# Optimization experiments

Measured on AMD Instinct MI355X. Metric: run time of the kernel, lower is better.

## Reference

```python
import jax, jax.numpy as jnp
import numpy as np

BN_EPS = 1e-5


def _gin_layer(x, src, dst, ew, eps, Wa, ba, Wb, bb, gamma, beta):
    # scatter-add aggregation: sum_j w_ij * x_j into node i
    msg = x[src] * ew[:, None]                       # [E, F]
    agg = jax.ops.segment_sum(msg, dst, num_segments=x.shape[0])  # [N, F]
    h = (1.0 + eps) * x + agg
    # MLP: Linear -> ReLU -> Linear -> BN(batch stats) -> ReLU
    h = jax.nn.relu(h @ Wa + ba)
    h = h @ Wb + bb
    mean = jnp.mean(h, axis=0)
    var = jnp.var(h, axis=0)
    h = (h - mean) * jax.lax.rsqrt(var + BN_EPS) * gamma + beta
    return jax.nn.relu(h)


def setup_inputs() -> dict:
    key = jax.random.key(0)
    N, E, F, H, L = 100000, 1600000, 128, 64, 3
    ks = jax.random.split(key, 12)
    x = jax.random.normal(ks[0], (N, F), dtype=jnp.float32)
    edge_index = jax.random.randint(ks[1], (2, E), 0, N, dtype=jnp.int64)
    edge_weight = jax.random.uniform(ks[2], (E,), dtype=jnp.float32)
    s = 0.05
    return {
        "x": x,
        "edge_index": edge_index,
        "edge_weight": edge_weight,
        # layer 1 (in_features -> hidden)
        "eps1": jnp.zeros((), jnp.float32),
        "W1a": jax.random.normal(ks[3], (F, H), jnp.float32) * s,
        "b1a": jnp.zeros((H,), jnp.float32),
        "W1b": jax.random.normal(ks[4], (H, H), jnp.float32) * s,
        "b1b": jnp.zeros((H,), jnp.float32),
        "g1": jnp.ones((H,), jnp.float32),
        "be1": jnp.zeros((H,), jnp.float32),
        # layers 2..L (hidden -> hidden), stacked on leading axis
        "epss": jnp.zeros((L - 1,), jnp.float32),
        "Wsa": jax.random.normal(ks[5], (L - 1, H, H), jnp.float32) * s,
        "bsa": jnp.zeros((L - 1, H), jnp.float32),
        "Wsb": jax.random.normal(ks[6], (L - 1, H, H), jnp.float32) * s,
        "bsb": jnp.zeros((L - 1, H), jnp.float32),
        "gs": jnp.ones((L - 1, H), jnp.float32),
        "bes": jnp.zeros((L - 1, H), jnp.float32),
    }


def reference(x, edge_index, edge_weight, eps1, W1a, b1a, W1b, b1b, g1, be1,
              epss, Wsa, bsa, Wsb, bsb, gs, bes):
    src, dst = edge_index[0], edge_index[1]
    h = _gin_layer(x, src, dst, edge_weight, eps1, W1a, b1a, W1b, b1b, g1, be1)
    for i in range(Wsa.shape[0]):
        h_new = _gin_layer(h, src, dst, edge_weight, epss[i],
                           Wsa[i], bsa[i], Wsb[i], bsb[i], gs[i], bes[i])
        h = h + h_new  # residual merge
    return h
```

## Files before the change

### kernel.cpp

```cpp
#include <hip/hip_runtime.h>

#define BN_EPS 1e-5f

typedef __attribute__((ext_vector_type(8))) short bf16x8;
typedef __attribute__((ext_vector_type(4))) float f32x4;

__device__ __forceinline__ unsigned short f32_to_bf16(float f) {
    unsigned u = __float_as_uint(f);
    u += 0x7fffu + ((u >> 16) & 1u);
    return (unsigned short)(u >> 16);
}
__device__ __forceinline__ float bf16_lo(unsigned v) { return __uint_as_float(v << 16); }
__device__ __forceinline__ float bf16_hi(unsigned v) { return __uint_as_float(v & 0xffff0000u); }

#define EW_SCALE (1.0f / 32767.0f)

__global__ __launch_bounds__(256) void scan_part1(
    const int* __restrict__ deg, int* __restrict__ blockSums, int N)
{
    __shared__ int sm[256];
    int t = threadIdx.x;
    int i0 = blockIdx.x * 512 + t * 2;
    int a = (i0     < N) ? deg[i0]     : 0;
    int b = (i0 + 1 < N) ? deg[i0 + 1] : 0;
    sm[t] = a + b;
    __syncthreads();
    for (int off = 128; off > 0; off >>= 1) {
        if (t < off) sm[t] += sm[t + off];
        __syncthreads();
    }
    if (t == 0) blockSums[blockIdx.x] = sm[0];
}

__global__ __launch_bounds__(256) void scan_part3(
    const int* __restrict__ deg, const int* __restrict__ blockSums,
    int* __restrict__ row_start, int NB, int N, int E)
{
    __shared__ int sb[256];
    __shared__ int sm[256];
    int t = threadIdx.x;

    sb[t] = (t < NB) ? blockSums[t] : 0;
    __syncthreads();
    for (int off = 1; off < 256; off <<= 1) {
        int v = (t >= off) ? sb[t - off] : 0;
        __syncthreads();
        sb[t] += v;
        __syncthreads();
    }
    const int boff = (blockIdx.x > 0) ? sb[blockIdx.x - 1] : 0;

    int i0 = blockIdx.x * 512 + t * 2;
    int a = (i0     < N) ? deg[i0]     : 0;
    int b = (i0 + 1 < N) ? deg[i0 + 1] : 0;
    sm[t] = a + b;
    __syncthreads();
    for (int off = 1; off < 256; off <<= 1) {
        int v = (t >= off) ? sm[t - off] : 0;
        __syncthreads();
        sm[t] += v;
        __syncthreads();
    }
    int excl = boff + ((t > 0) ? sm[t - 1] : 0);
    if (i0 < N)     row_start[i0]     = excl;
    if (i0 + 1 < N) row_start[i0 + 1] = excl + a;
    if (blockIdx.x == 0 && t == 0) row_start[N] = E;
}

__global__ __launch_bounds__(256) void fill_pass2(
    const int* __restrict__ src, const int* __restrict__ dst,
    const float* __restrict__ ew, const int* __restrict__ rank,
    const int* __restrict__ row_start, unsigned* __restrict__ einfo, int E)
{
    int i = blockIdx.x * 256 + threadIdx.x;
    if (i < E) {
        int pos = row_start[dst[i]] + rank[i];
        unsigned q = (unsigned)__float2int_rn(ew[i] * 32767.0f);
        einfo[pos] = ((unsigned)src[i] << 15) | q;
    }
}

__global__ __launch_bounds__(256) void prep_wfrag(
    const float* __restrict__ W1a, const float* __restrict__ W1b,
    const float* __restrict__ Wsa, const float* __restrict__ Wsb,
    unsigned short* __restrict__ wf, int* __restrict__ deg,
    float* __restrict__ stats3, int N, int nW)
{
    int z = blockIdx.x * 256 + threadIdx.x;
    if (z < N) deg[z] = 0;
    if (z < 384) stats3[z] = 0.f;

    int bid = blockIdx.x;
    if (bid >= nW) return;
    const float* src; unsigned short* dst; int KS, chunk;
    if (bid < 4)      { src = W1a; dst = wf;        KS = 4; chunk = bid; }
    else if (bid < 6) { src = W1b; dst = wf + 8192; KS = 2; chunk = bid - 4; }
    else {
        int t = bid - 6;
        int layer = t >> 2;
        int wh = (t >> 1) & 1;
        chunk = t & 1;
        src = (wh ? Wsb : Wsa) + (size_t)layer * 4096;
        dst = wf + 12288 + layer * 8192 + wh * 4096;
        KS = 2;
    }
    int base = chunk * 2048;
    for (int e = base + threadIdx.x; e < base + 2048; e += 256) {
        int j  = e & 7;
        int l  = (e >> 3) & 63;
        int nk = e >> 9;
        int ks = nk % KS, n = nk / KS;
        int k  = ks * 32 + ((l >> 4) << 3) + j;
        int c  = n * 16 + (l & 15);
        dst[e] = f32_to_bf16(src[k * 64 + c]);
    }
}

template<int KS, int MODE, bool BF16OUT, bool STATS>
__global__ __launch_bounds__(256) void gemm_mfma(
    const void* __restrict__ Ain, const unsigned short* __restrict__ wfrag,
    const float* __restrict__ bias, void* __restrict__ out,
    float* __restrict__ statsOut,
    const float* __restrict__ statsIn, const float* __restrict__ g,
    const float* __restrict__ be, const float* __restrict__ res,
    float* __restrict__ hout, int N,
    const int* __restrict__ rdst, int* __restrict__ rdeg,
    int* __restrict__ rrank, int rE, int gblocks)
{
    constexpr int K   = KS * 32;
    constexpr int LDA = K + 8;
    __shared__ __align__(16) unsigned short sA[64 * LDA];
    __shared__ float sab[128];

    const int tid = threadIdx.x;
    if ((int)blockIdx.x >= gblocks) {
        int i = (blockIdx.x - gblocks) * 256 + tid;
        if (i < rE) rrank[i] = atomicAdd(&rdeg[rdst[i]], 1);
        return;
    }
    const int bid = blockIdx.x;

    if (MODE == 2) {
        if (tid < 64) {
            float invN = 1.0f / (float)N;
            float mean = statsIn[tid] * invN;
            float var  = statsIn[64 + tid] * invN - mean * mean;
            float a = g[tid] * rsqrtf(var + BN_EPS);
            sab[tid]      = a;
            sab[64 + tid] = be[tid] - mean * a;
        }
        __syncthreads();
    }

    const int w  = tid >> 6;
    const int l  = tid & 63;
    const int lr = l & 15;
    const int lg = l >> 4;
    const int ntiles = (N + 63) >> 6;
    const bf16x8* wg = (const bf16x8*)wfrag;

    float csAcc[4] = {0.f, 0.f, 0.f, 0.f};
    float cqAcc[4] = {0.f, 0.f, 0.f, 0.f};

    for (int tile = bid; tile < ntiles; tile += gblocks) {
        const int r0 = tile * 64;

        if (MODE == 1) {
            const uint4* Au = (const uint4*)Ain;
            constexpr int C16 = K / 8;
            for (int i = tid; i < 64 * C16; i += 256) {
                int r = i / C16, c = i % C16;
                uint4 v = make_uint4(0u, 0u, 0u, 0u);
                if (r0 + r < N) v = Au[(size_t)(r0 + r) * C16 + c];
                *reinterpret_cast<uint4*>(&sA[r * LDA + c * 8]) = v;
            }
        } else {
            const float* Af = (const float*)Ain;
            constexpr int C4 = K / 4;
            for (int i = tid; i < 64 * C4; i += 256) {
                int r = i / C4, c4 = i % C4;
                int gr = r0 + r;
                float4 v = make_float4(0.f, 0.f, 0.f, 0.f);
                if (gr < N) {
                    v = reinterpret_cast<const float4*>(Af + (size_t)gr * K)[c4];
                    if (MODE == 2) {
                        int l0 = c4 * 4;
                        v.x = fmaxf(fmaf(v.x, sab[l0 + 0], sab[64 + l0 + 0]), 0.f);
                        v.y = fmaxf(fmaf(v.y, sab[l0 + 1], sab[64 + l0 + 1]), 0.f);
                        v.z = fmaxf(fmaf(v.z, sab[l0 + 2], sab[64 + l0 + 2]), 0.f);
                        v.w = fmaxf(fmaf(v.w, sab[l0 + 3], sab[64 + l0 + 3]), 0.f);
                        if (res) {
                            float4 rv = reinterpret_cast<const float4*>(res + (size_t)gr * K)[c4];
                            v.x += rv.x; v.y += rv.y; v.z += rv.z; v.w += rv.w;
                        }
                        reinterpret_cast<float4*>(hout + (size_t)gr * K)[c4] = v;
                    }
                }
                ushort4 pk;
                pk.x = f32_to_bf16(v.x); pk.y = f32_to_bf16(v.y);
                pk.z = f32_to_bf16(v.z); pk.w = f32_to_bf16(v.w);
                *reinterpret_cast<ushort4*>(&sA[r * LDA + c4 * 4]) = pk;
            }
        }
        __syncthreads();

        f32x4 acc0 = {0.f,0.f,0.f,0.f}, acc1 = {0.f,0.f,0.f,0.f};
        f32x4 acc2 = {0.f,0.f,0.f,0.f}, acc3 = {0.f,0.f,0.f,0.f};

        #pragma unroll
        for (int ks = 0; ks < KS; ++ks) {
            bf16x8 af = *reinterpret_cast<const bf16x8*>(
                &sA[(w * 16 + lr) * LDA + ks * 32 + lg * 8]);
            bf16x8 b0 = wg[(0 * KS + ks) * 64 + l];
            bf16x8 b1 = wg[(1 * KS + ks) * 64 + l];
            bf16x8 b2 = wg[(2 * KS + ks) * 64 + l];
            bf16x8 b3 = wg[(3 * KS + ks) * 64 + l];
            acc0 = __builtin_amdgcn_mfma_f32_16x16x32_bf16(af, b0, acc0, 0, 0, 0);
            acc1 = __builtin_amdgcn_mfma_f32_16x16x32_bf16(af, b1, acc1, 0, 0, 0);
            acc2 = __builtin_amdgcn_mfma_f32_16x16x32_bf16(af, b2, acc2, 0, 0, 0);
            acc3 = __builtin_amdgcn_mfma_f32_16x16x32_bf16(af, b3, acc3, 0, 0, 0);
        }

        const int rlocal = w * 16 + lg * 4;
        float v[4][4];
        #pragma unroll
        for (int n = 0; n < 4; ++n) {
            float bv = bias ? bias[n * 16 + lr] : 0.f;
            f32x4 a = (n == 0) ? acc0 : (n == 1) ? acc1 : (n == 2) ? acc2 : acc3;
            #pragma unroll
            for (int j = 0; j < 4; ++j) {
                float vv = a[j] + bv;
                v[n][j] = vv;
                if (STATS && (r0 + rlocal + j < N)) {
                    csAcc[n] += vv; cqAcc[n] += vv * vv;
                }
            }
        }

        __syncthreads();

        if (BF16OUT) {
            #pragma unroll
            for (int n = 0; n < 4; ++n)
                #pragma unroll
                for (int j = 0; j < 4; ++j)
                    sA[(rlocal + j) * 72 + n * 16 + lr] = f32_to_bf16(v[n][j]);
            __syncthreads();
            unsigned short* o = (unsigned short*)out;
            for (int i = tid; i < 64 * 8; i += 256) {
                int r = i >> 3, q = i & 7;
                if (r0 + r < N)
                    *reinterpret_cast<uint4*>(o + (size_t)(r0 + r) * 64 + q * 8) =
                        *reinterpret_cast<const uint4*>(&sA[r * 72 + q * 8]);
            }
        } else {
            float* o = (float*)out;
            float* sAf = reinterpret_cast<float*>(sA);
            #pragma unroll
            for (int half = 0; half < 2; ++half) {
                if ((w >> 1) == half) {
                    #pragma unroll
                    for (int n = 0; n < 4; ++n)
                        #pragma unroll
                        for (int j = 0; j < 4; ++j)
                            sAf[((w & 1) * 16 + lg * 4 + j) * 68 + n * 16 + lr] = v[n][j];
                }
                __syncthreads();
                for (int i = tid; i < 32 * 16; i += 256) {
                    int r = i >> 4, c4 = i & 15;
                    int gr = r0 + half * 32 + r;
                    if (gr < N)
                        *reinterpret_cast<float4*>(o + (size_t)gr * 64 + c4 * 4) =
                            *reinterpret_cast<const float4*>(&sAf[r * 68 + c4 * 4]);
                }
                __syncthreads();
            }
        }
        __syncthreads();
    }

    if (STATS) {
        float* red = reinterpret_cast<float*>(sA);
        int gg = w * 4 + lg;
        #pragma unroll
        for (int n = 0; n < 4; ++n) red[gg * 64 + n * 16 + lr] = csAcc[n];
        __syncthreads();
        if (tid < 64) {
            float s = 0.f;
            #pragma unroll
            for (int g2 = 0; g2 < 16; ++g2) s += red[g2 * 64 + tid];
            atomicAdd(&statsOut[tid], s);
        }
        __syncthreads();
        #pragma unroll
        for (int n = 0; n < 4; ++n) red[gg * 64 + n * 16 + lr] = cqAcc[n];
        __syncthreads();
        if (tid < 64) {
            float q = 0.f;
            #pragma unroll
            for (int g2 = 0; g2 < 16; ++g2) q += red[g2 * 64 + tid];
            atomicAdd(&statsOut[64 + tid], q);
        }
    }
}

__global__ __launch_bounds__(256) void aggmid_kernel(
    const unsigned* __restrict__ yu,
    const int* __restrict__ row_start,
    const unsigned* __restrict__ einfo,
    const float* __restrict__ epsp,
    const float* __restrict__ ba,
    unsigned* __restrict__ midu, int N)
{
    const int lane = threadIdx.x & 63;
    const int q    = lane >> 4;
    const int u    = lane & 15;
    int w  = (blockIdx.x * 256 + threadIdx.x) >> 6;
    const int nw = (gridDim.x * 256) >> 6;
    const float eps1 = 1.0f + epsp[0];
    const float4 bal = *reinterpret_cast<const float4*>(ba + 4 * u);

    for (int r = w; r < N; r += nw) {
        const int rs = row_start[r];
        const int re = row_start[r + 1];

        float A0=0.f,A1=0.f,A2=0.f,A3=0.f, B0=0.f,B1=0.f,B2=0.f,B3=0.f;
        float C0=0.f,C1=0.f,C2=0.f,C3=0.f, D0=0.f,D1=0.f,D2=0.f,D3=0.f;
        int j = rs;
        for (; j + 16 <= re; j += 16) {
            const int b = j + q * 4;
            unsigned p0 = einfo[b + 0], p1 = einfo[b + 1];
            unsigned p2 = einfo[b + 2], p3 = einfo[b + 3];
            uint2 y0 = *reinterpret_cast<const uint2*>(&yu[(size_t)(p0 >> 15) * 32 + 2 * u]);
            uint2 y1 = *reinterpret_cast<const uint2*>(&yu[(size_t)(p1 >> 15) * 32 + 2 * u]);
            uint2 y2 = *reinterpret_cast<const uint2*>(&yu[(size_t)(p2 >> 15) * 32 + 2 * u]);
            uint2 y3 = *reinterpret_cast<const uint2*>(&yu[(size_t)(p3 >> 15) * 32 + 2 * u]);
            float w0 = (float)(p0 & 0x7FFFu) * EW_SCALE;
            float w1 = (float)(p1 & 0x7FFFu) * EW_SCALE;
            float w2 = (float)(p2 & 0x7FFFu) * EW_SCALE;
            float w3 = (float)(p3 & 0x7FFFu) * EW_SCALE;
            A0 = fmaf(w0, bf16_lo(y0.x), A0); A1 = fmaf(w0, bf16_hi(y0.x), A1);
            A2 = fmaf(w0, bf16_lo(y0.y), A2); A3 = fmaf(w0, bf16_hi(y0.y), A3);
            B0 = fmaf(w1, bf16_lo(y1.x), B0); B1 = fmaf(w1, bf16_hi(y1.x), B1);
            B2 = fmaf(w1, bf16_lo(y1.y), B2); B3 = fmaf(w1, bf16_hi(y1.y), B3);
            C0 = fmaf(w2, bf16_lo(y2.x), C0); C1 = fmaf(w2, bf16_hi(y2.x), C1);
            C2 = fmaf(w2, bf16_lo(y2.y), C2); C3 = fmaf(w2, bf16_hi(y2.y), C3);
            D0 = fmaf(w3, bf16_lo(y3.x), D0); D1 = fmaf(w3, bf16_hi(y3.x), D1);
            D2 = fmaf(w3, bf16_lo(y3.y), D2); D3 = fmaf(w3, bf16_hi(y3.y), D3);
        }
        for (; j + 4 <= re; j += 4) {
            unsigned p = einfo[j + q];
            uint2 y = *reinterpret_cast<const uint2*>(&yu[(size_t)(p >> 15) * 32 + 2 * u]);
            float wv = (float)(p & 0x7FFFu) * EW_SCALE;
            A0 = fmaf(wv, bf16_lo(y.x), A0); A1 = fmaf(wv, bf16_hi(y.x), A1);
            A2 = fmaf(wv, bf16_lo(y.y), A2); A3 = fmaf(wv, bf16_hi(y.y), A3);
        }
        if (j < re) {
            int e = j + q;
            bool valid = e < re;
            unsigned p = einfo[valid ? e : rs];
            float wv = valid ? (float)(p & 0x7FFFu) * EW_SCALE : 0.f;
            uint2 y = *reinterpret_cast<const uint2*>(&yu[(size_t)(p >> 15) * 32 + 2 * u]);
            B0 = fmaf(wv, bf16_lo(y.x), B0); B1 = fmaf(wv, bf16_hi(y.x), B1);
            B2 = fmaf(wv, bf16_lo(y.y), B2); B3 = fmaf(wv, bf16_hi(y.y), B3);
        }
        float s0 = (A0 + B0) + (C0 + D0);
        float s1 = (A1 + B1) + (C1 + D1);
        float s2 = (A2 + B2) + (C2 + D2);
        float s3 = (A3 + B3) + (C3 + D3);
        s0 += __shfl_xor(s0, 16); s0 += __shfl_xor(s0, 32);
        s1 += __shfl_xor(s1, 16); s1 += __shfl_xor(s1, 32);
        s2 += __shfl_xor(s2, 16); s2 += __shfl_xor(s2, 32);
        s3 += __shfl_xor(s3, 16); s3 += __shfl_xor(s3, 32);

        uint2 sv = *reinterpret_cast<const uint2*>(&yu[(size_t)r * 32 + 2 * u]);
        float m0 = fmaf(eps1, bf16_lo(sv.x), s0) + bal.x;
        float m1 = fmaf(eps1, bf16_hi(sv.x), s1) + bal.y;
        float m2 = fmaf(eps1, bf16_lo(sv.y), s2) + bal.z;
        float m3 = fmaf(eps1, bf16_hi(sv.y), s3) + bal.w;
        if (q == 0) {
            uint2 pk;
            pk.x = (unsigned)f32_to_bf16(fmaxf(m0, 0.f))
                 | ((unsigned)f32_to_bf16(fmaxf(m1, 0.f)) << 16);
            pk.y = (unsigned)f32_to_bf16(fmaxf(m2, 0.f))
                 | ((unsigned)f32_to_bf16(fmaxf(m3, 0.f)) << 16);
            *reinterpret_cast<uint2*>(&midu[(size_t)r * 32 + 2 * u]) = pk;
        }
    }
}

template<int RES>
__global__ __launch_bounds__(256) void bn_apply(
    const float* __restrict__ h2, const float* __restrict__ stats,
    const float* __restrict__ g, const float* __restrict__ be,
    const float* res, float* out, int N, int n4)
{
    __shared__ float sab[128];
    int t = threadIdx.x;
    if (t < 64) {
        float invN = 1.0f / (float)N;
        float mean = stats[t] * invN;
        float var  = stats[64 + t] * invN - mean * mean;
        float a = g[t] * rsqrtf(var + BN_EPS);
        sab[t]      = a;
        sab[64 + t] = be[t] - mean * a;
    }
    __syncthreads();

    int i = blockIdx.x * blockDim.x + t;
    int stride = gridDim.x * blockDim.x;
    for (; i < n4; i += stride) {
        float4 v = reinterpret_cast<const float4*>(h2)[i];
        int l0 = (i * 4) & 63;
        float4 o;
        o.x = fmaxf(fmaf(v.x, sab[l0 + 0], sab[64 + l0 + 0]), 0.f);
        o.y = fmaxf(fmaf(v.y, sab[l0 + 1], sab[64 + l0 + 1]), 0.f);
        o.z = fmaxf(fmaf(v.z, sab[l0 + 2], sab[64 + l0 + 2]), 0.f);
        o.w = fmaxf(fmaf(v.w, sab[l0 + 3], sab[64 + l0 + 3]), 0.f);
        if (RES) {
            float4 rv = reinterpret_cast<const float4*>(res)[i];
            o.x += rv.x; o.y += rv.y; o.z += rv.z; o.w += rv.w;
        }
        reinterpret_cast<float4*>(out)[i] = o;
    }
}

extern "C" void kernel_launch(void* const* d_in, const int* in_sizes, int n_in,
                              void* d_out, int out_size, void* d_ws, size_t ws_size,
                              hipStream_t stream)
{
    const float* x    = (const float*)d_in[0];
    const int*   ei   = (const int*)  d_in[1];
    const float* ew   = (const float*)d_in[2];
    const float* eps1 = (const float*)d_in[3];
    const float* W1a  = (const float*)d_in[4];
    const float* b1a  = (const float*)d_in[5];
    const float* W1b  = (const float*)d_in[6];
    const float* b1b  = (const float*)d_in[7];
    const float* g1   = (const float*)d_in[8];
    const float* be1  = (const float*)d_in[9];
    const float* epss = (const float*)d_in[10];
    const float* Wsa  = (const float*)d_in[11];
    const float* bsa  = (const float*)d_in[12];
    const float* Wsb  = (const float*)d_in[13];
    const float* bsb  = (const float*)d_in[14];
    const float* gs   = (const float*)d_in[15];
    const float* bes  = (const float*)d_in[16];

    const int N   = in_sizes[0] / 128;
    const int E   = in_sizes[2];
    const int Lm1 = in_sizes[10];
    const int* src  = ei;
    const int* dstp = ei + E;

    char* ws = (char*)d_ws;
    size_t off = 0;
    unsigned* einfo = (unsigned*)(ws + off); off += (size_t)E * 4;
    float* regA  = (float*)(ws + off);   off += (size_t)N * 128 * 4;
    unsigned* ybf = (unsigned*)(ws + off); off += (size_t)N * 32 * 4;
    int*   rank  = (int*)  (ws + off);   off += (size_t)E * 4;
    int*   deg   = (int*)  (ws + off);   off += (size_t)N * 4;
    int*   row_start = (int*)(ws + off); off += (size_t)(N + 1) * 4;
    float* stats3 = (float*)(ws + off);  off += 384 * 4;
    int*   blockSums = (int*)(ws + off); off += 256 * 4;
    off = (off + 15) & ~(size_t)15;
    unsigned short* wf = (unsigned short*)(ws + off);
    float* outp  = (float*)d_out;
    float* bufY  = regA;
    unsigned* midu = (unsigned*)(regA + (size_t)N * 64);

    const int n4   = N * 64 / 4;
    const int NB   = (N + 511) / 512;
    const int EB   = (E + 255) / 256;
    const int nW   = 6 + 4 * Lm1;
    const int PREP_B = (N + 255) / 256;
    const int NT   = (N + 63) / 64;
    const int GBS  = 1024;

    prep_wfrag<<<PREP_B, 256, 0, stream>>>(W1a, W1b, Wsa, Wsb, wf, deg, stats3, N, nW);

    gemm_mfma<4, 0, true, false><<<1024 + EB, 256, 0, stream>>>(
        x, wf, nullptr, ybf, nullptr, nullptr, nullptr, nullptr, nullptr, nullptr, N,
        dstp, deg, rank, E, 1024);

    scan_part1<<<NB, 256, 0, stream>>>(deg, blockSums, N);
    scan_part3<<<NB, 256, 0, stream>>>(deg, blockSums, row_start, NB, N, E);
    fill_pass2<<<EB, 256, 0, stream>>>(src, dstp, ew, rank, row_start, einfo, E);

    aggmid_kernel<<<2048, 256, 0, stream>>>(ybf, row_start, einfo, eps1, b1a, midu, N);
    gemm_mfma<2, 1, false, true><<<GBS, 256, 0, stream>>>(
        midu, wf + 8192, b1b, bufY, stats3, nullptr, nullptr, nullptr, nullptr, nullptr, N,
        nullptr, nullptr, nullptr, 0, GBS);

    const float* pg  = g1;
    const float* pbe = be1;
    const float* resp = nullptr;
    for (int i = 0; i < Lm1; ++i) {
        const unsigned short* wfAi = wf + 12288 + i * 8192;
        const unsigned short* wfBi = wf + 12288 + i * 8192 + 4096;
        gemm_mfma<2, 2, true, false><<<NT, 256, 0, stream>>>(
            bufY, wfAi, nullptr, ybf, nullptr, stats3 + i * 128, pg, pbe, resp, outp, N,
            nullptr, nullptr, nullptr, 0, NT);
        aggmid_kernel<<<2048, 256, 0, stream>>>(
            ybf, row_start, einfo, epss + i, bsa + (size_t)i * 64, midu, N);
        gemm_mfma<2, 1, false, true><<<GBS, 256, 0, stream>>>(
            midu, wfBi, bsb + (size_t)i * 64, bufY, stats3 + (i + 1) * 128,
            nullptr, nullptr, nullptr, nullptr, nullptr, N,
            nullptr, nullptr, nullptr, 0, GBS);
        pg  = gs  + (size_t)i * 64;
        pbe = bes + (size_t)i * 64;
        resp = outp;
    }

    if (Lm1 > 0)
        bn_apply<1><<<2048, 256, 0, stream>>>(bufY, stats3 + Lm1 * 128, pg, pbe, outp, outp, N, n4);
    else
        bn_apply<0><<<2048, 256, 0, stream>>>(bufY, stats3, pg, pbe, nullptr, outp, N, n4);
}
```

Before: 401.5 us.

## Fuse second MLP linear and BN stats into aggregation kernel

New measurement: 544.9 us. 35.7% more time.

```diff
diff --git a/kernel.cpp b/kernel.cpp
--- a/kernel.cpp
+++ b/kernel.cpp
@@ -81,8 +81,7 @@
 }
 
 __global__ __launch_bounds__(256) void prep_wfrag(
-    const float* __restrict__ W1a, const float* __restrict__ W1b,
-    const float* __restrict__ Wsa, const float* __restrict__ Wsb,
+    const float* __restrict__ W1a, const float* __restrict__ Wsa,
     unsigned short* __restrict__ wf, int* __restrict__ deg,
     float* __restrict__ stats3, int N, int nW)
 {
@@ -93,15 +92,13 @@
     int bid = blockIdx.x;
     if (bid >= nW) return;
     const float* src; unsigned short* dst; int KS, chunk;
-    if (bid < 4)      { src = W1a; dst = wf;        KS = 4; chunk = bid; }
-    else if (bid < 6) { src = W1b; dst = wf + 8192; KS = 2; chunk = bid - 4; }
+    if (bid < 4) { src = W1a; dst = wf; KS = 4; chunk = bid; }
     else {
-        int t = bid - 6;
-        int layer = t >> 2;
-        int wh = (t >> 1) & 1;
+        int t = bid - 4;
+        int layer = t >> 1;
         chunk = t & 1;
-        src = (wh ? Wsb : Wsa) + (size_t)layer * 4096;
-        dst = wf + 12288 + layer * 8192 + wh * 4096;
+        src = Wsa + (size_t)layer * 4096;
+        dst = wf + 8192 + layer * 4096;
         KS = 2;
     }
     int base = chunk * 2048;
@@ -116,11 +113,10 @@
     }
 }
 
-template<int KS, int MODE, bool BF16OUT, bool STATS>
+template<int KS, int MODE>
 __global__ __launch_bounds__(256) void gemm_mfma(
     const void* __restrict__ Ain, const unsigned short* __restrict__ wfrag,
-    const float* __restrict__ bias, void* __restrict__ out,
-    float* __restrict__ statsOut,
+    void* __restrict__ out,
     const float* __restrict__ statsIn, const float* __restrict__ g,
     const float* __restrict__ be, const float* __restrict__ res,
     float* __restrict__ hout, int N,
@@ -159,22 +155,10 @@
     const int ntiles = (N + 63) >> 6;
     const bf16x8* wg = (const bf16x8*)wfrag;
 
-    float csAcc[4] = {0.f, 0.f, 0.f, 0.f};
-    float cqAcc[4] = {0.f, 0.f, 0.f, 0.f};
-
     for (int tile = bid; tile < ntiles; tile += gblocks) {
         const int r0 = tile * 64;
 
-        if (MODE == 1) {
-            const uint4* Au = (const uint4*)Ain;
-            constexpr int C16 = K / 8;
-            for (int i = tid; i < 64 * C16; i += 256) {
-                int r = i / C16, c = i % C16;
-                uint4 v = make_uint4(0u, 0u, 0u, 0u);
-                if (r0 + r < N) v = Au[(size_t)(r0 + r) * C16 + c];
-                *reinterpret_cast<uint4*>(&sA[r * LDA + c * 8]) = v;
-            }
-        } else {
+        {
             const float* Af = (const float*)Ain;
             constexpr int C4 = K / 4;
             for (int i = tid; i < 64 * C4; i += 256) {
@@ -225,100 +209,62 @@
         float v[4][4];
         #pragma unroll
         for (int n = 0; n < 4; ++n) {
-            float bv = bias ? bias[n * 16 + lr] : 0.f;
             f32x4 a = (n == 0) ? acc0 : (n == 1) ? acc1 : (n == 2) ? acc2 : acc3;
             #pragma unroll
-            for (int j = 0; j < 4; ++j) {
-                float vv = a[j] + bv;
-                v[n][j] = vv;
-                if (STATS && (r0 + rlocal + j < N)) {
-                    csAcc[n] += vv; cqAcc[n] += vv * vv;
-                }
-            }
-        }
-
-        __syncthreads();
-
-        if (BF16OUT) {
+            for (int j = 0; j < 4; ++j) v[n][j] = a[j];
+        }
+
+        __syncthreads();
+
+        #pragma unroll
+        for (int n = 0; n < 4; ++n)
             #pragma unroll
-            for (int n = 0; n < 4; ++n)
-                #pragma unroll
-                for (int j = 0; j < 4; ++j)
-                    sA[(rlocal + j) * 72 + n * 16 + lr] = f32_to_bf16(v[n][j]);
-            __syncthreads();
-            unsigned short* o = (unsigned short*)out;
-            for (int i = tid; i < 64 * 8; i += 256) {
-                int r = i >> 3, q = i & 7;
-                if (r0 + r < N)
-                    *reinterpret_cast<uint4*>(o + (size_t)(r0 + r) * 64 + q * 8) =
-                        *reinterpret_cast<const uint4*>(&sA[r * 72 + q * 8]);
-            }
-        } else {
-            float* o = (float*)out;
-            float* sAf = reinterpret_cast<float*>(sA);
-            #pragma unroll
-            for (int half = 0; half < 2; ++half) {
-                if ((w >> 1) == half) {
-                    #pragma unroll
-                    for (int n = 0; n < 4; ++n)
-                        #pragma unroll
-                        for (int j = 0; j < 4; ++j)
-                            sAf[((w & 1) * 16 + lg * 4 + j) * 68 + n * 16 + lr] = v[n][j];
-                }
-                __syncthreads();
-                for (int i = tid; i < 32 * 16; i += 256) {
-                    int r = i >> 4, c4 = i & 15;
-                    int gr = r0 + half * 32 + r;
-                    if (gr < N)
-                        *reinterpret_cast<float4*>(o + (size_t)gr * 64 + c4 * 4) =
-                            *reinterpret_cast<const float4*>(&sAf[r * 68 + c4 * 4]);
-                }
-                __syncthreads();
-            }
-        }
-        __syncthreads();
-    }
-
-    if (STATS) {
-        float* red = reinterpret_cast<float*>(sA);
-        int gg = w * 4 + lg;
-        #pragma unroll
-        for (int n = 0; n < 4; ++n) red[gg * 64 + n * 16 + lr] = csAcc[n];
-        __syncthreads();
-        if (tid < 64) {
-            float s = 0.f;
-            #pragma unroll
-            for (int g2 = 0; g2 < 16; ++g2) s += red[g2 * 64 + tid];
-            atomicAdd(&statsOut[tid], s);
-        }
-        __syncthreads();
-        #pragma unroll
-        for (int n = 0; n < 4; ++n) red[gg * 64 + n * 16 + lr] = cqAcc[n];
-        __syncthreads();
-        if (tid < 64) {
-            float q = 0.f;
-            #pragma unroll
-            for (int g2 = 0; g2 < 16; ++g2) q += red[g2 * 64 + tid];
-            atomicAdd(&statsOut[64 + tid], q);
-        }
-    }
-}
-
-__global__ __launch_bounds__(256) void aggmid_kernel(
+            for (int j = 0; j < 4; ++j)
+                sA[(rlocal + j) * 72 + n * 16 + lr] = f32_to_bf16(v[n][j]);
+        __syncthreads();
+        unsigned short* o = (unsigned short*)out;
+        for (int i = tid; i < 64 * 8; i += 256) {
+            int r = i >> 3, q = i & 7;
+            if (r0 + r < N)
+                *reinterpret_cast<uint4*>(o + (size_t)(r0 + r) * 64 + q * 8) =
+                    *reinterpret_cast<const uint4*>(&sA[r * 72 + q * 8]);
+        }
+        __syncthreads();
+    }
+}
+
+__global__ __launch_bounds__(256) void agg_mlp_kernel(
     const unsigned* __restrict__ yu,
     const int* __restrict__ row_start,
     const unsigned* __restrict__ einfo,
     const float* __restrict__ epsp,
     const float* __restrict__ ba,
-    unsigned* __restrict__ midu, int N)
-{
-    const int lane = threadIdx.x & 63;
+    const float* __restrict__ Wb,
+    const float* __restrict__ bb,
+    float* __restrict__ h2out,
+    float* __restrict__ statsOut, int N)
+{
+    __shared__ float sWb[64 * 64];
+    __shared__ float rowbuf[4][64];
+    __shared__ float sred[4][64];
+
+    const int tid  = threadIdx.x;
+    const int lane = tid & 63;
+    const int wid  = tid >> 6;
     const int q    = lane >> 4;
     const int u    = lane & 15;
-    int w  = (blockIdx.x * 256 + threadIdx.x) >> 6;
+
+    for (int i = tid; i < 1024; i += 256)
+        reinterpret_cast<float4*>(sWb)[i] = reinterpret_cast<const float4*>(Wb)[i];
+    __syncthreads();
+
+    int w  = (blockIdx.x * 256 + tid) >> 6;
     const int nw = (gridDim.x * 256) >> 6;
     const float eps1 = 1.0f + epsp[0];
     const float4 bal = *reinterpret_cast<const float4*>(ba + 4 * u);
+    const float bb_l = bb[lane];
+
+    float csA = 0.f, cqA = 0.f;
 
     for (int r = w; r < N; r += nw) {
         const int rs = row_start[r];
@@ -374,18 +320,42 @@
         s3 += __shfl_xor(s3, 16); s3 += __shfl_xor(s3, 32);
 
         uint2 sv = *reinterpret_cast<const uint2*>(&yu[(size_t)r * 32 + 2 * u]);
-        float m0 = fmaf(eps1, bf16_lo(sv.x), s0) + bal.x;
-        float m1 = fmaf(eps1, bf16_hi(sv.x), s1) + bal.y;
-        float m2 = fmaf(eps1, bf16_lo(sv.y), s2) + bal.z;
-        float m3 = fmaf(eps1, bf16_hi(sv.y), s3) + bal.w;
-        if (q == 0) {
-            uint2 pk;
-            pk.x = (unsigned)f32_to_bf16(fmaxf(m0, 0.f))
-                 | ((unsigned)f32_to_bf16(fmaxf(m1, 0.f)) << 16);
-            pk.y = (unsigned)f32_to_bf16(fmaxf(m2, 0.f))
-                 | ((unsigned)f32_to_bf16(fmaxf(m3, 0.f)) << 16);
-            *reinterpret_cast<uint2*>(&midu[(size_t)r * 32 + 2 * u]) = pk;
-        }
+        float m0 = fmaxf(fmaf(eps1, bf16_lo(sv.x), s0) + bal.x, 0.f);
+        float m1 = fmaxf(fmaf(eps1, bf16_hi(sv.x), s1) + bal.y, 0.f);
+        float m2 = fmaxf(fmaf(eps1, bf16_lo(sv.y), s2) + bal.z, 0.f);
+        float m3 = fmaxf(fmaf(eps1, bf16_hi(sv.y), s3) + bal.w, 0.f);
+
+        if (q == 0)
+            *reinterpret_cast<float4*>(&rowbuf[wid][4 * u]) =
+                make_float4(m0, m1, m2, m3);
+
+        float acc = bb_l;
+        #pragma unroll 4
+        for (int k = 0; k < 64; k += 4) {
+            float4 m = *reinterpret_cast<const float4*>(&rowbuf[wid][k]);
+            acc = fmaf(m.x, sWb[(k + 0) * 64 + lane], acc);
+            acc = fmaf(m.y, sWb[(k + 1) * 64 + lane], acc);
+            acc = fmaf(m.z, sWb[(k + 2) * 64 + lane], acc);
+            acc = fmaf(m.w, sWb[(k + 3) * 64 + lane], acc);
+        }
+        h2out[(size_t)r * 64 + lane] = acc;
+        csA += acc;
+        cqA += acc * acc;
+    }
+
+    __syncthreads();
+    sred[wid][lane] = csA;
+    __syncthreads();
+    if (tid < 64) {
+        float s = sred[0][tid] + sred[1][tid] + sred[2][tid] + sred[3][tid];
+        atomicAdd(&statsOut[tid], s);
+    }
+    __syncthreads();
+    sred[wid][lane] = cqA;
+    __syncthreads();
+    if (tid < 64) {
+        float qq = sred[0][tid] + sred[1][tid] + sred[2][tid] + sred[3][tid];
+        atomicAdd(&statsOut[64 + tid], qq);
     }
 }
 
@@ -467,46 +437,39 @@
     unsigned short* wf = (unsigned short*)(ws + off);
     float* outp  = (float*)d_out;
     float* bufY  = regA;
-    unsigned* midu = (unsigned*)(regA + (size_t)N * 64);
 
     const int n4   = N * 64 / 4;
     const int NB   = (N + 511) / 512;
     const int EB   = (E + 255) / 256;
-    const int nW   = 6 + 4 * Lm1;
+    const int nW   = 4 + 2 * Lm1;
     const int PREP_B = (N + 255) / 256;
     const int NT   = (N + 63) / 64;
-    const int GBS  = 1024;
-
-    prep_wfrag<<<PREP_B, 256, 0, stream>>>(W1a, W1b, Wsa, Wsb, wf, deg, stats3, N, nW);
-
-    gemm_mfma<4, 0, true, false><<<1024 + EB, 256, 0, stream>>>(
-        x, wf, nullptr, ybf, nullptr, nullptr, nullptr, nullptr, nullptr, nullptr, N,
+
+    prep_wfrag<<<PREP_B, 256, 0, stream>>>(W1a, Wsa, wf, deg, stats3, N, nW);
+
+    gemm_mfma<4, 0><<<1024 + EB, 256, 0, stream>>>(
+        x, wf, ybf, nullptr, nullptr, nullptr, nullptr, nullptr, N,
         dstp, deg, rank, E, 1024);
 
     scan_part1<<<NB, 256, 0, stream>>>(deg, blockSums, N);
     scan_part3<<<NB, 256, 0, stream>>>(deg, blockSums, row_start, NB, N, E);
     fill_pass2<<<EB, 256, 0, stream>>>(src, dstp, ew, rank, row_start, einfo, E);
 
-    aggmid_kernel<<<2048, 256, 0, stream>>>(ybf, row_start, einfo, eps1, b1a, midu, N);
-    gemm_mfma<2, 1, false, true><<<GBS, 256, 0, stream>>>(
-        midu, wf + 8192, b1b, bufY, stats3, nullptr, nullptr, nullptr, nullptr, nullptr, N,
-        nullptr, nullptr, nullptr, 0, GBS);
+    agg_mlp_kernel<<<2048, 256, 0, stream>>>(
+        ybf, row_start, einfo, eps1, b1a, W1b, b1b, bufY, stats3, N);
 
     const float* pg  = g1;
     const float* pbe = be1;
     const float* resp = nullptr;
     for (int i = 0; i < Lm1; ++i) {
-        const unsigned short* wfAi = wf + 12288 + i * 8192;
-        const unsigned short* wfBi = wf + 12288 + i * 8192 + 4096;
-        gemm_mfma<2, 2, true, false><<<NT, 256, 0, stream>>>(
-            bufY, wfAi, nullptr, ybf, nullptr, stats3 + i * 128, pg, pbe, resp, outp, N,
+        const unsigned short* wfAi = wf + 8192 + i * 4096;
+        gemm_mfma<2, 2><<<NT, 256, 0, stream>>>(
+            bufY, wfAi, ybf, stats3 + i * 128, pg, pbe, resp, outp, N,
             nullptr, nullptr, nullptr, 0, NT);
-        aggmid_kernel<<<2048, 256, 0, stream>>>(
-            ybf, row_start, einfo, epss + i, bsa + (size_t)i * 64, midu, N);
-        gemm_mfma<2, 1, false, true><<<GBS, 256, 0, stream>>>(
-            midu, wfBi, bsb + (size_t)i * 64, bufY, stats3 + (i + 1) * 128,
-            nullptr, nullptr, nullptr, nullptr, nullptr, N,
-            nullptr, nullptr, nullptr, 0, GBS);
+        agg_mlp_kernel<<<2048, 256, 0, stream>>>(
+            ybf, row_start, einfo, epss + i, bsa + (size_t)i * 64,
+            Wsb + (size_t)i * 64 * 64, bsb + (size_t)i * 64,
+            bufY, stats3 + (i + 1) * 128, N);
         pg  = gs  + (size_t)i * 64;
         pbe = bes + (size_t)i * 64;
         resp = outp;
```

## Fuse scan and CSR fill into one kernel with software grid barriers

Applied to the files above, without the earlier changes.

After: 462.0 us. 1.15x slower.

```diff
diff --git a/kernel.cpp b/kernel.cpp
--- a/kernel.cpp
+++ b/kernel.cpp
@@ -15,66 +15,76 @@
 
 #define EW_SCALE (1.0f / 32767.0f)
 
-__global__ __launch_bounds__(256) void scan_part1(
-    const int* __restrict__ deg, int* __restrict__ blockSums, int N)
+__global__ __launch_bounds__(256) void scan_fill(
+    const int* __restrict__ deg, int* __restrict__ blockSums,
+    int* __restrict__ row_start,
+    const int* __restrict__ src, const int* __restrict__ dstp,
+    const float* __restrict__ ew, const int* __restrict__ rank,
+    unsigned* __restrict__ einfo, int* __restrict__ bar,
+    int NB, int N, int E, int GB)
 {
     __shared__ int sm[256];
-    int t = threadIdx.x;
-    int i0 = blockIdx.x * 512 + t * 2;
-    int a = (i0     < N) ? deg[i0]     : 0;
-    int b = (i0 + 1 < N) ? deg[i0 + 1] : 0;
-    sm[t] = a + b;
+    __shared__ int sb[256];
+    const int t = threadIdx.x;
+    const int b = blockIdx.x;
+
+    if (b < NB) {
+        int i0 = b * 512 + t * 2;
+        int a = (i0     < N) ? deg[i0]     : 0;
+        int c = (i0 + 1 < N) ? deg[i0 + 1] : 0;
+        sm[t] = a + c;
+        __syncthreads();
+        for (int off = 128; off > 0; off >>= 1) {
+            if (t < off) sm[t] += sm[t + off];
+            __syncthreads();
+        }
+        if (t == 0) blockSums[b] = sm[0];
+    }
     __syncthreads();
-    for (int off = 128; off > 0; off >>= 1) {
-        if (t < off) sm[t] += sm[t + off];
-        __syncthreads();
-    }
-    if (t == 0) blockSums[blockIdx.x] = sm[0];
-}
-
-__global__ __launch_bounds__(256) void scan_part3(
-    const int* __restrict__ deg, const int* __restrict__ blockSums,
-    int* __restrict__ row_start, int NB, int N, int E)
-{
-    __shared__ int sb[256];
-    __shared__ int sm[256];
-    int t = threadIdx.x;
-
-    sb[t] = (t < NB) ? blockSums[t] : 0;
+    if (t == 0) {
+        __threadfence();
+        atomicAdd(bar, 1);
+        while (atomicAdd(bar, 0) < GB) __builtin_amdgcn_s_sleep(2);
+    }
     __syncthreads();
-    for (int off = 1; off < 256; off <<= 1) {
-        int v = (t >= off) ? sb[t - off] : 0;
-        __syncthreads();
-        sb[t] += v;
-        __syncthreads();
-    }
-    const int boff = (blockIdx.x > 0) ? sb[blockIdx.x - 1] : 0;
-
-    int i0 = blockIdx.x * 512 + t * 2;
-    int a = (i0     < N) ? deg[i0]     : 0;
-    int b = (i0 + 1 < N) ? deg[i0 + 1] : 0;
-    sm[t] = a + b;
+
+    if (b < NB) {
+        sb[t] = (t < NB) ? blockSums[t] : 0;
+        __syncthreads();
+        for (int off = 1; off < 256; off <<= 1) {
+            int v = (t >= off) ? sb[t - off] : 0;
+            __syncthreads();
+            sb[t] += v;
+            __syncthreads();
+        }
+        const int boff = (b > 0) ? sb[b - 1] : 0;
+
+        int i0 = b * 512 + t * 2;
+        int a = (i0     < N) ? deg[i0]     : 0;
+        int c = (i0 + 1 < N) ? deg[i0 + 1] : 0;
+        sm[t] = a + c;
+        __syncthreads();
+        for (int off = 1; off < 256; off <<= 1) {
+            int v = (t >= off) ? sm[t - off] : 0;
+            __syncthreads();
+            sm[t] += v;
+            __syncthreads();
+        }
+        int excl = boff + ((t > 0) ? sm[t - 1] : 0);
+        if (i0 < N)     row_start[i0]     = excl;
+        if (i0 + 1 < N) row_start[i0 + 1] = excl + a;
+        if (b == 0 && t == 0) row_start[N] = E;
+    }
     __syncthreads();
-    for (int off = 1; off < 256; off <<= 1) {
-        int v = (t >= off) ? sm[t - off] : 0;
-        __syncthreads();
-        sm[t] += v;
-        __syncthreads();
-    }
-    int excl = boff + ((t > 0) ? sm[t - 1] : 0);
-    if (i0 < N)     row_start[i0]     = excl;
-    if (i0 + 1 < N) row_start[i0 + 1] = excl + a;
-    if (blockIdx.x == 0 && t == 0) row_start[N] = E;
-}
-
-__global__ __launch_bounds__(256) void fill_pass2(
-    const int* __restrict__ src, const int* __restrict__ dst,
-    const float* __restrict__ ew, const int* __restrict__ rank,
-    const int* __restrict__ row_start, unsigned* __restrict__ einfo, int E)
-{
-    int i = blockIdx.x * 256 + threadIdx.x;
-    if (i < E) {
-        int pos = row_start[dst[i]] + rank[i];
+    if (t == 0) {
+        __threadfence();
+        atomicAdd(bar, 1);
+        while (atomicAdd(bar, 0) < 2 * GB) __builtin_amdgcn_s_sleep(2);
+    }
+    __syncthreads();
+
+    for (int i = b * 256 + t; i < E; i += GB * 256) {
+        int pos = row_start[dstp[i]] + rank[i];
         unsigned q = (unsigned)__float2int_rn(ew[i] * 32767.0f);
         einfo[pos] = ((unsigned)src[i] << 15) | q;
     }
@@ -84,11 +94,12 @@
     const float* __restrict__ W1a, const float* __restrict__ W1b,
     const float* __restrict__ Wsa, const float* __restrict__ Wsb,
     unsigned short* __restrict__ wf, int* __restrict__ deg,
-    float* __restrict__ stats3, int N, int nW)
+    float* __restrict__ stats3, int* __restrict__ bar, int N, int nW)
 {
     int z = blockIdx.x * 256 + threadIdx.x;
     if (z < N) deg[z] = 0;
     if (z < 384) stats3[z] = 0.f;
+    if (z == 0) bar[0] = 0;
 
     int bid = blockIdx.x;
     if (bid >= nW) return;
@@ -463,6 +474,7 @@
     int*   row_start = (int*)(ws + off); off += (size_t)(N + 1) * 4;
     float* stats3 = (float*)(ws + off);  off += 384 * 4;
     int*   blockSums = (int*)(ws + off); off += 256 * 4;
+    int*   bar = (int*)(ws + off);       off += 16;
     off = (off + 15) & ~(size_t)15;
     unsigned short* wf = (unsigned short*)(ws + off);
     float* outp  = (float*)d_out;
@@ -476,16 +488,17 @@
     const int PREP_B = (N + 255) / 256;
     const int NT   = (N + 63) / 64;
     const int GBS  = 1024;
-
-    prep_wfrag<<<PREP_B, 256, 0, stream>>>(W1a, W1b, Wsa, Wsb, wf, deg, stats3, N, nW);
+    const int SFB  = 512;
+
+    prep_wfrag<<<PREP_B, 256, 0, stream>>>(W1a, W1b, Wsa, Wsb, wf, deg, stats3, bar, N, nW);
 
     gemm_mfma<4, 0, true, false><<<1024 + EB, 256, 0, stream>>>(
         x, wf, nullptr, ybf, nullptr, nullptr, nullptr, nullptr, nullptr, nullptr, N,
         dstp, deg, rank, E, 1024);
 
-    scan_part1<<<NB, 256, 0, stream>>>(deg, blockSums, N);
-    scan_part3<<<NB, 256, 0, stream>>>(deg, blockSums, row_start, NB, N, E);
-    fill_pass2<<<EB, 256, 0, stream>>>(src, dstp, ew, rank, row_start, einfo, E);
+    scan_fill<<<SFB, 256, 0, stream>>>(deg, blockSums, row_start,
+                                       src, dstp, ew, rank, einfo, bar,
+                                       NB, N, E, SFB);
 
     aggmid_kernel<<<2048, 256, 0, stream>>>(ybf, row_start, einfo, eps1, b1a, midu, N);
     gemm_mfma<2, 1, false, true><<<GBS, 256, 0, stream>>>(
```
